# Optimization experiments

Measured on AMD Instinct MI355X. Metric: run time of the kernel, lower is better.

Reference implementation:

```python
import jax, jax.numpy as jnp
import numpy as np

TOP_K = 2
NUM_EXPERTS = 64


def setup_inputs() -> dict:
    key = jax.random.key(0)
    k1, k2 = jax.random.split(key)
    hidden_states = jax.random.normal(k1, (4, 4096, 2048), dtype=jnp.float32)
    gate_weight = jax.random.normal(k2, (NUM_EXPERTS, 2048), dtype=jnp.float32) * 0.02
    return {"hidden_states": hidden_states, "gate_weight": gate_weight}


def reference(hidden_states, gate_weight):
    B, S, D = hidden_states.shape
    E = gate_weight.shape[0]
    num_tokens = B * S
    x = hidden_states.reshape(num_tokens, D)
    # gate: Linear(d_model, num_experts, bias=False)
    gate_logits = jnp.einsum('td,ed->te', x, gate_weight)  # [T, E]
    gate_probs = jax.nn.softmax(gate_logits, axis=-1)
    top_k_probs, top_k_indices = jax.lax.top_k(gate_probs, TOP_K)
    # normalize_gates=True
    top_k_probs = top_k_probs / jnp.sum(top_k_probs, axis=-1, keepdims=True)
    # histogram of expert assignments (replaces the python loop over experts)
    tokens_per_expert = jax.ops.segment_sum(
        jnp.ones((num_tokens * TOP_K,), dtype=jnp.float32),
        top_k_indices.reshape(-1),
        num_segments=E,
    )
    # auxiliary load-balancing loss
    fraction_per_expert = tokens_per_expert / num_tokens
    mean_gate_probs = jnp.mean(gate_probs, axis=0)
    aux_loss = jnp.sum(fraction_per_expert * mean_gate_probs) * E
    return top_k_probs, top_k_indices, tokens_per_expert, aux_loss
```

## Files before the change

kernel.cpp:

```cpp
#include <hip/hip_runtime.h>
#include <hip/hip_bf16.h>

#define TOKENS   16384
#define DMODEL   2048
#define NEXP     64
#define BK       64
#define TB       32
#define TT       8

#define OFF_IDX  (TOKENS * 2)
#define OFF_HIST (TOKENS * 4)
#define OFF_AUX  (TOKENS * 4 + NEXP)

__global__ __launch_bounds__(256) void router_kernel(
    const float* __restrict__ x,
    const float* __restrict__ gw,
    float* __restrict__ out,
    float* __restrict__ probsum_g,
    float* __restrict__ hist_g)
{
    __shared__ float xs[TB][BK];
    __shared__ float wt[BK][NEXP + 1];
    __shared__ float psum_s[4][NEXP];
    __shared__ int   hist_s[NEXP];

    const int tid  = threadIdx.x;
    const int wave = tid >> 6;
    const int lane = tid & 63;
    const int tok0 = blockIdx.x * TB;

    if (tid < NEXP) hist_s[tid] = 0;

    float acc[TT];
#pragma unroll
    for (int t = 0; t < TT; ++t) acc[t] = 0.f;

    for (int k0 = 0; k0 < DMODEL; k0 += BK) {
        __syncthreads();
#pragma unroll
        for (int i = 0; i < (TB * BK / 4) / 256; ++i) {
            int idx = tid + i * 256;
            int r = idx >> 4;
            int c = idx & 15;
            *(float4*)&xs[r][c * 4] =
                *(const float4*)&x[(size_t)(tok0 + r) * DMODEL + k0 + c * 4];
        }
#pragma unroll
        for (int i = 0; i < 4; ++i) {
            int idx = tid + i * 256;
            int e = idx >> 4;
            int c = idx & 15;
            float4 v = *(const float4*)&gw[(size_t)e * DMODEL + k0 + c * 4];
            wt[c * 4 + 0][e] = v.x;
            wt[c * 4 + 1][e] = v.y;
            wt[c * 4 + 2][e] = v.z;
            wt[c * 4 + 3][e] = v.w;
        }
        __syncthreads();

#pragma unroll
        for (int kk4 = 0; kk4 < BK / 4; ++kk4) {
            float w0 = wt[kk4 * 4 + 0][lane];
            float w1 = wt[kk4 * 4 + 1][lane];
            float w2 = wt[kk4 * 4 + 2][lane];
            float w3 = wt[kk4 * 4 + 3][lane];
#pragma unroll
            for (int t = 0; t < TT; ++t) {
                float4 xv = *(const float4*)&xs[wave * TT + t][kk4 * 4];
                acc[t] = fmaf(xv.x, w0, acc[t]);
                acc[t] = fmaf(xv.y, w1, acc[t]);
                acc[t] = fmaf(xv.z, w2, acc[t]);
                acc[t] = fmaf(xv.w, w3, acc[t]);
            }
        }
    }

    float local_psum = 0.f;
    const int tokA = tok0 + wave * TT;

#pragma unroll
    for (int t = 0; t < TT; ++t) {
        float v = acc[t];
        float m = v;
#pragma unroll
        for (int off = 32; off; off >>= 1) m = fmaxf(m, __shfl_xor(m, off));
        float ex = __expf(v - m);
        float S = ex;
#pragma unroll
        for (int off = 32; off; off >>= 1) S += __shfl_xor(S, off);
        local_psum += ex / S;

        float bv = v; int bi = lane;
#pragma unroll
        for (int off = 32; off; off >>= 1) {
            float ov = __shfl_xor(bv, off);
            int   oi = __shfl_xor(bi, off);
            if (ov > bv || (ov == bv && oi < bi)) { bv = ov; bi = oi; }
        }
        float v1 = bv; int i1 = bi;
        float bv2 = (lane == i1) ? -3.4e38f : v; int bi2 = lane;
#pragma unroll
        for (int off = 32; off; off >>= 1) {
            float ov = __shfl_xor(bv2, off);
            int   oi = __shfl_xor(bi2, off);
            if (ov > bv2 || (ov == bv2 && oi < bi2)) { bv2 = ov; bi2 = oi; }
        }
        float v2 = bv2; int i2 = bi2;

        if (lane == 0) {
            float e1 = __expf(v1 - m);
            float e2 = __expf(v2 - m);
            float inv = 1.f / (e1 + e2);
            int tok = tokA + t;
            out[tok * 2 + 0] = e1 * inv;
            out[tok * 2 + 1] = e2 * inv;
            out[OFF_IDX + tok * 2 + 0] = (float)i1;
            out[OFF_IDX + tok * 2 + 1] = (float)i2;
            atomicAdd(&hist_s[i1], 1);
            atomicAdd(&hist_s[i2], 1);
        }
    }

    psum_s[wave][lane] = local_psum;
    __syncthreads();
    if (wave == 0) {
        float s = psum_s[0][lane] + psum_s[1][lane] + psum_s[2][lane] + psum_s[3][lane];
        atomicAdd(&probsum_g[lane], s);
        atomicAdd(&hist_g[lane], (float)hist_s[lane]);
    }
}

__global__ void finalize_kernel(const float* __restrict__ probsum_g,
                                const float* __restrict__ hist_g,
                                float* __restrict__ out)
{
    int e = threadIdx.x;
    float tpe = hist_g[e];
    out[OFF_HIST + e] = tpe;
    const float invT = 1.f / (float)TOKENS;
    float term = (tpe * invT) * (probsum_g[e] * invT);
#pragma unroll
    for (int off = 32; off; off >>= 1) term += __shfl_xor(term, off);
    if (e == 0) out[OFF_AUX] = term * (float)NEXP;
}

extern "C" void kernel_launch(void* const* d_in, const int* in_sizes, int n_in,
                              void* d_out, int out_size, void* d_ws, size_t ws_size,
                              hipStream_t stream) {
    const float* x  = (const float*)d_in[0];
    const float* gw = (const float*)d_in[1];
    float* out = (float*)d_out;
    float* ws  = (float*)d_ws;

    hipMemsetAsync(d_ws, 0, 128 * sizeof(float), stream);

    dim3 grid(TOKENS / TB);
    router_kernel<<<grid, 256, 0, stream>>>(x, gw, out, ws, ws + NEXP);
    finalize_kernel<<<1, 64, 0, stream>>>(ws, ws + NEXP, out);
}
```

Before: 210.8 us.

## Restructure router GEMM: lane-per-token, wave-uniform weight loads, double-buffered x tiles

Each lane now owns a token and each wave owns 8 experts, so gate weights are read as wave-uniform (scalar-friendly) global loads instead of being transposed into shared memory. x tiles of 64 tokens are double-buffered with register prefetch, and logits are transposed through shared memory for the softmax and top-2 stage. Blocks grow to 512 threads with 64 tokens each. This removes the shared-memory weight transpose and cuts LDS traffic per FMA. The cost is per-iteration global weight reads and an extra shared-memory transpose step.

```diff
diff --git a/kernel.cpp b/kernel.cpp
--- a/kernel.cpp
+++ b/kernel.cpp
@@ -4,24 +4,25 @@
 #define TOKENS   16384
 #define DMODEL   2048
 #define NEXP     64
-#define BK       64
-#define TB       32
-#define TT       8
+#define KW       64
+#define NIT      (DMODEL / KW)
+#define TB       64
+#define PAD      68
 
 #define OFF_IDX  (TOKENS * 2)
 #define OFF_HIST (TOKENS * 4)
 #define OFF_AUX  (TOKENS * 4 + NEXP)
 
-__global__ __launch_bounds__(256) void router_kernel(
+__global__ __launch_bounds__(512) void router_kernel(
     const float* __restrict__ x,
     const float* __restrict__ gw,
     float* __restrict__ out,
     float* __restrict__ probsum_g,
     float* __restrict__ hist_g)
 {
-    __shared__ float xs[TB][BK];
-    __shared__ float wt[BK][NEXP + 1];
-    __shared__ float psum_s[4][NEXP];
+    __shared__ float xs[2][TB][PAD];
+    __shared__ float ls[TB][PAD];
+    __shared__ float psum_s[8][NEXP];
     __shared__ int   hist_s[NEXP];
 
     const int tid  = threadIdx.x;
@@ -31,56 +32,66 @@
 
     if (tid < NEXP) hist_s[tid] = 0;
 
-    float acc[TT];
+    const int e0 = __builtin_amdgcn_readfirstlane(wave << 3);
+
+    const float4* wr[8];
 #pragma unroll
-    for (int t = 0; t < TT; ++t) acc[t] = 0.f;
+    for (int j = 0; j < 8; ++j)
+        wr[j] = (const float4*)(gw + (size_t)(e0 + j) * DMODEL);
 
-    for (int k0 = 0; k0 < DMODEL; k0 += BK) {
-        __syncthreads();
+    float acc[8];
 #pragma unroll
-        for (int i = 0; i < (TB * BK / 4) / 256; ++i) {
-            int idx = tid + i * 256;
-            int r = idx >> 4;
-            int c = idx & 15;
-            *(float4*)&xs[r][c * 4] =
-                *(const float4*)&x[(size_t)(tok0 + r) * DMODEL + k0 + c * 4];
-        }
-#pragma unroll
-        for (int i = 0; i < 4; ++i) {
-            int idx = tid + i * 256;
-            int e = idx >> 4;
-            int c = idx & 15;
-            float4 v = *(const float4*)&gw[(size_t)e * DMODEL + k0 + c * 4];
-            wt[c * 4 + 0][e] = v.x;
-            wt[c * 4 + 1][e] = v.y;
-            wt[c * 4 + 2][e] = v.z;
-            wt[c * 4 + 3][e] = v.w;
+    for (int j = 0; j < 8; ++j) acc[j] = 0.f;
+
+    const int sr = tid >> 3;
+    const int sc = (tid & 7) * 8;
+    const float* xrow = x + (size_t)(tok0 + sr) * DMODEL + sc;
+
+    float4 ra = *(const float4*)(xrow);
+    float4 rb = *(const float4*)(xrow + 4);
+    *(float4*)&xs[0][sr][sc]     = ra;
+    *(float4*)&xs[0][sr][sc + 4] = rb;
+    ra = *(const float4*)(xrow + KW);
+    rb = *(const float4*)(xrow + KW + 4);
+
+    for (int it = 0; it < NIT; ++it) {
+        const int cur = it & 1;
+        if (it + 1 < NIT) {
+            *(float4*)&xs[cur ^ 1][sr][sc]     = ra;
+            *(float4*)&xs[cur ^ 1][sr][sc + 4] = rb;
+            if (it + 2 < NIT) {
+                ra = *(const float4*)(xrow + (size_t)(it + 2) * KW);
+                rb = *(const float4*)(xrow + (size_t)(it + 2) * KW + 4);
+            }
         }
         __syncthreads();
 
+        const float* xl = &xs[cur][lane][0];
+        const int kbase = (it * KW) >> 2;
+#pragma unroll 4
+        for (int kk = 0; kk < KW / 4; ++kk) {
+            float4 xv = *(const float4*)(xl + kk * 4);
 #pragma unroll
-        for (int kk4 = 0; kk4 < BK / 4; ++kk4) {
-            float w0 = wt[kk4 * 4 + 0][lane];
-            float w1 = wt[kk4 * 4 + 1][lane];
-            float w2 = wt[kk4 * 4 + 2][lane];
-            float w3 = wt[kk4 * 4 + 3][lane];
-#pragma unroll
-            for (int t = 0; t < TT; ++t) {
-                float4 xv = *(const float4*)&xs[wave * TT + t][kk4 * 4];
-                acc[t] = fmaf(xv.x, w0, acc[t]);
-                acc[t] = fmaf(xv.y, w1, acc[t]);
-                acc[t] = fmaf(xv.z, w2, acc[t]);
-                acc[t] = fmaf(xv.w, w3, acc[t]);
+            for (int j = 0; j < 8; ++j) {
+                float4 wv = wr[j][kbase + kk];
+                acc[j] = fmaf(xv.x, wv.x, acc[j]);
+                acc[j] = fmaf(xv.y, wv.y, acc[j]);
+                acc[j] = fmaf(xv.z, wv.z, acc[j]);
+                acc[j] = fmaf(xv.w, wv.w, acc[j]);
             }
         }
+        __syncthreads();
     }
 
+    *(float4*)&ls[lane][e0]     = make_float4(acc[0], acc[1], acc[2], acc[3]);
+    *(float4*)&ls[lane][e0 + 4] = make_float4(acc[4], acc[5], acc[6], acc[7]);
+    __syncthreads();
+
     float local_psum = 0.f;
-    const int tokA = tok0 + wave * TT;
-
 #pragma unroll
-    for (int t = 0; t < TT; ++t) {
-        float v = acc[t];
+    for (int t = 0; t < 8; ++t) {
+        const int tl = wave * 8 + t;
+        float v = ls[tl][lane];
         float m = v;
 #pragma unroll
         for (int off = 32; off; off >>= 1) m = fmaxf(m, __shfl_xor(m, off));
@@ -111,7 +122,7 @@
             float e1 = __expf(v1 - m);
             float e2 = __expf(v2 - m);
             float inv = 1.f / (e1 + e2);
-            int tok = tokA + t;
+            int tok = tok0 + tl;
             out[tok * 2 + 0] = e1 * inv;
             out[tok * 2 + 1] = e2 * inv;
             out[OFF_IDX + tok * 2 + 0] = (float)i1;
@@ -124,7 +135,9 @@
     psum_s[wave][lane] = local_psum;
     __syncthreads();
     if (wave == 0) {
-        float s = psum_s[0][lane] + psum_s[1][lane] + psum_s[2][lane] + psum_s[3][lane];
+        float s = 0.f;
+#pragma unroll
+        for (int i = 0; i < 8; ++i) s += psum_s[i][lane];
         atomicAdd(&probsum_g[lane], s);
         atomicAdd(&hist_g[lane], (float)hist_s[lane]);
     }
@@ -155,6 +168,6 @@
     hipMemsetAsync(d_ws, 0, 128 * sizeof(float), stream);
 
     dim3 grid(TOKENS / TB);
-    router_kernel<<<grid, 256, 0, stream>>>(x, gw, out, ws, ws + NEXP);
+    router_kernel<<<grid, 512, 0, stream>>>(x, gw, out, ws, ws + NEXP);
     finalize_kernel<<<1, 64, 0, stream>>>(ws, ws + NEXP, out);
 }
```

New measurement: 238.1 us. +12.9%, slower.

## Replace LDS-tiled gate GEMM with register-pipelined direct global loads

Applied to the files above, without the earlier changes.

Removes the shared-memory tiles and per-tile barriers. Each wave now streams its 8 token rows and a per-lane weight column straight from global memory into four rotating register banks, so loads for later chunks are in flight while FMAs run on earlier ones. Scalar prefetch loads touch rows ahead of use, and a separate kernel re-lays the gate weights into a chunk-major layout in workspace so each chunk's weight load is coalesced. This trades LDS traffic and barriers for higher register pressure and broadcast x loads. It also adds an extra kernel launch per call.

```diff
diff --git a/kernel.cpp b/kernel.cpp
--- a/kernel.cpp
+++ b/kernel.cpp
@@ -1,85 +1,146 @@
 #include <hip/hip_runtime.h>
 #include <hip/hip_bf16.h>
 
-#define TOKENS   16384
-#define DMODEL   2048
-#define NEXP     64
-#define BK       64
-#define TB       32
-#define TT       8
+#define TOKENS 16384
+#define DMODEL 2048
+#define NEXP   64
+#define NCH    (DMODEL / 4)
+#define NWIN   32
+#define TPB    32
+#define TPW    8
 
 #define OFF_IDX  (TOKENS * 2)
 #define OFF_HIST (TOKENS * 4)
 #define OFF_AUX  (TOKENS * 4 + NEXP)
 
-__global__ __launch_bounds__(256) void router_kernel(
+#define W4_FLOATS (DMODEL * NEXP)
+
+__global__ __launch_bounds__(256) void transpose_w(const float* __restrict__ gw,
+                                                   float* __restrict__ w4)
+{
+    int idx = blockIdx.x * 256 + threadIdx.x;
+    int e  = idx & 63;
+    int k4 = idx >> 6;
+    float4 v = *(const float4*)(gw + (size_t)e * DMODEL + k4 * 4);
+    *(float4*)(w4 + (size_t)idx * 4) = v;
+}
+
+struct Bank {
+    float4 r0, r1, r2, r3, r4, r5, r6, r7;
+    float4 w;
+};
+
+template<bool USE_W4>
+__global__ __launch_bounds__(256, 2) void router_kernel(
     const float* __restrict__ x,
     const float* __restrict__ gw,
+    const float* __restrict__ w4,
     float* __restrict__ out,
     float* __restrict__ probsum_g,
     float* __restrict__ hist_g)
 {
-    __shared__ float xs[TB][BK];
-    __shared__ float wt[BK][NEXP + 1];
     __shared__ float psum_s[4][NEXP];
     __shared__ int   hist_s[NEXP];
 
     const int tid  = threadIdx.x;
     const int wave = tid >> 6;
     const int lane = tid & 63;
-    const int tok0 = blockIdx.x * TB;
+    const int tko  = __builtin_amdgcn_readfirstlane((int)(blockIdx.x * TPB) + wave * TPW);
 
     if (tid < NEXP) hist_s[tid] = 0;
 
-    float acc[TT];
-#pragma unroll
-    for (int t = 0; t < TT; ++t) acc[t] = 0.f;
-
-    for (int k0 = 0; k0 < DMODEL; k0 += BK) {
-        __syncthreads();
-#pragma unroll
-        for (int i = 0; i < (TB * BK / 4) / 256; ++i) {
-            int idx = tid + i * 256;
-            int r = idx >> 4;
-            int c = idx & 15;
-            *(float4*)&xs[r][c * 4] =
-                *(const float4*)&x[(size_t)(tok0 + r) * DMODEL + k0 + c * 4];
-        }
-#pragma unroll
-        for (int i = 0; i < 4; ++i) {
-            int idx = tid + i * 256;
-            int e = idx >> 4;
-            int c = idx & 15;
-            float4 v = *(const float4*)&gw[(size_t)e * DMODEL + k0 + c * 4];
-            wt[c * 4 + 0][e] = v.x;
-            wt[c * 4 + 1][e] = v.y;
-            wt[c * 4 + 2][e] = v.z;
-            wt[c * 4 + 3][e] = v.w;
-        }
-        __syncthreads();
-
-#pragma unroll
-        for (int kk4 = 0; kk4 < BK / 4; ++kk4) {
-            float w0 = wt[kk4 * 4 + 0][lane];
-            float w1 = wt[kk4 * 4 + 1][lane];
-            float w2 = wt[kk4 * 4 + 2][lane];
-            float w3 = wt[kk4 * 4 + 3][lane];
-#pragma unroll
-            for (int t = 0; t < TT; ++t) {
-                float4 xv = *(const float4*)&xs[wave * TT + t][kk4 * 4];
-                acc[t] = fmaf(xv.x, w0, acc[t]);
-                acc[t] = fmaf(xv.y, w1, acc[t]);
-                acc[t] = fmaf(xv.z, w2, acc[t]);
-                acc[t] = fmaf(xv.w, w3, acc[t]);
-            }
-        }
-    }
+    int lz;
+    asm("v_mov_b32 %0, 0" : "=v"(lz));
+
+    const float* xp0 = x + (size_t)(tko + 0) * DMODEL;
+    const float* xp1 = x + (size_t)(tko + 1) * DMODEL;
+    const float* xp2 = x + (size_t)(tko + 2) * DMODEL;
+    const float* xp3 = x + (size_t)(tko + 3) * DMODEL;
+    const float* xp4 = x + (size_t)(tko + 4) * DMODEL;
+    const float* xp5 = x + (size_t)(tko + 5) * DMODEL;
+    const float* xp6 = x + (size_t)(tko + 6) * DMODEL;
+    const float* xp7 = x + (size_t)(tko + 7) * DMODEL;
+    const float* gwd = gw + (size_t)lane * DMODEL;
+
+    float acc[8];
+#pragma unroll
+    for (int t = 0; t < 8; ++t) acc[t] = 0.f;
+
+    auto LOADB = [&](Bank& B, int C) __attribute__((always_inline)) {
+        B.r0 = *(const float4*)(xp0 + lz + (size_t)C * 4);
+        B.r1 = *(const float4*)(xp1 + lz + (size_t)C * 4);
+        B.r2 = *(const float4*)(xp2 + lz + (size_t)C * 4);
+        B.r3 = *(const float4*)(xp3 + lz + (size_t)C * 4);
+        B.r4 = *(const float4*)(xp4 + lz + (size_t)C * 4);
+        B.r5 = *(const float4*)(xp5 + lz + (size_t)C * 4);
+        B.r6 = *(const float4*)(xp6 + lz + (size_t)C * 4);
+        B.r7 = *(const float4*)(xp7 + lz + (size_t)C * 4);
+        B.w  = USE_W4 ? *(const float4*)(w4 + (size_t)C * (NEXP * 4) + (lane << 2))
+                      : *(const float4*)(gwd + (size_t)C * 4);
+    };
+
+    auto FMAB = [&](Bank& B) __attribute__((always_inline)) {
+        acc[0]=fmaf(B.r0.x,B.w.x,acc[0]); acc[0]=fmaf(B.r0.y,B.w.y,acc[0]);
+        acc[0]=fmaf(B.r0.z,B.w.z,acc[0]); acc[0]=fmaf(B.r0.w,B.w.w,acc[0]);
+        acc[1]=fmaf(B.r1.x,B.w.x,acc[1]); acc[1]=fmaf(B.r1.y,B.w.y,acc[1]);
+        acc[1]=fmaf(B.r1.z,B.w.z,acc[1]); acc[1]=fmaf(B.r1.w,B.w.w,acc[1]);
+        acc[2]=fmaf(B.r2.x,B.w.x,acc[2]); acc[2]=fmaf(B.r2.y,B.w.y,acc[2]);
+        acc[2]=fmaf(B.r2.z,B.w.z,acc[2]); acc[2]=fmaf(B.r2.w,B.w.w,acc[2]);
+        acc[3]=fmaf(B.r3.x,B.w.x,acc[3]); acc[3]=fmaf(B.r3.y,B.w.y,acc[3]);
+        acc[3]=fmaf(B.r3.z,B.w.z,acc[3]); acc[3]=fmaf(B.r3.w,B.w.w,acc[3]);
+        acc[4]=fmaf(B.r4.x,B.w.x,acc[4]); acc[4]=fmaf(B.r4.y,B.w.y,acc[4]);
+        acc[4]=fmaf(B.r4.z,B.w.z,acc[4]); acc[4]=fmaf(B.r4.w,B.w.w,acc[4]);
+        acc[5]=fmaf(B.r5.x,B.w.x,acc[5]); acc[5]=fmaf(B.r5.y,B.w.y,acc[5]);
+        acc[5]=fmaf(B.r5.z,B.w.z,acc[5]); acc[5]=fmaf(B.r5.w,B.w.w,acc[5]);
+        acc[6]=fmaf(B.r6.x,B.w.x,acc[6]); acc[6]=fmaf(B.r6.y,B.w.y,acc[6]);
+        acc[6]=fmaf(B.r6.z,B.w.z,acc[6]); acc[6]=fmaf(B.r6.w,B.w.w,acc[6]);
+        acc[7]=fmaf(B.r7.x,B.w.x,acc[7]); acc[7]=fmaf(B.r7.y,B.w.y,acc[7]);
+        acc[7]=fmaf(B.r7.z,B.w.z,acc[7]); acc[7]=fmaf(B.r7.w,B.w.w,acc[7]);
+    };
+
+    Bank A, B, C, D;
+
+    float pfa = x[(size_t)(tko + (lane >> 3)) * DMODEL + 0 * 64 + ((lane & 3) << 4)];
+    float pfb = x[(size_t)(tko + (lane >> 3)) * DMODEL + 1 * 64 + ((lane & 3) << 4)];
+
+    LOADB(A, 0); LOADB(B, 1); LOADB(C, 2); LOADB(D, 3);
+
+    for (int w = 0; w < NWIN - 1; ++w) {
+        const int c0 = w * 16;
+        float pfn = 0.f;
+        if (w + 2 < NWIN)
+            pfn = x[(size_t)(tko + (lane >> 3)) * DMODEL + (w + 2) * 64 + ((lane & 3) << 4)];
+
+        FMAB(A); LOADB(A, c0 + 4);   FMAB(B); LOADB(B, c0 + 5);
+        FMAB(C); LOADB(C, c0 + 6);   FMAB(D); LOADB(D, c0 + 7);
+        FMAB(A); LOADB(A, c0 + 8);   FMAB(B); LOADB(B, c0 + 9);
+        FMAB(C); LOADB(C, c0 + 10);  FMAB(D); LOADB(D, c0 + 11);
+        FMAB(A); LOADB(A, c0 + 12);  FMAB(B); LOADB(B, c0 + 13);
+        FMAB(C); LOADB(C, c0 + 14);  FMAB(D); LOADB(D, c0 + 15);
+        FMAB(A); LOADB(A, c0 + 16);  FMAB(B); LOADB(B, c0 + 17);
+        FMAB(C); LOADB(C, c0 + 18);  FMAB(D); LOADB(D, c0 + 19);
+
+        asm volatile("" :: "v"(pfa));
+        pfa = pfb; pfb = pfn;
+    }
+    {
+        const int c0 = (NWIN - 1) * 16;
+        FMAB(A); LOADB(A, c0 + 4);   FMAB(B); LOADB(B, c0 + 5);
+        FMAB(C); LOADB(C, c0 + 6);   FMAB(D); LOADB(D, c0 + 7);
+        FMAB(A); LOADB(A, c0 + 8);   FMAB(B); LOADB(B, c0 + 9);
+        FMAB(C); LOADB(C, c0 + 10);  FMAB(D); LOADB(D, c0 + 11);
+        FMAB(A); LOADB(A, c0 + 12);  FMAB(B); LOADB(B, c0 + 13);
+        FMAB(C); LOADB(C, c0 + 14);  FMAB(D); LOADB(D, c0 + 15);
+        FMAB(A); FMAB(B); FMAB(C); FMAB(D);
+        asm volatile("" :: "v"(pfa));
+        asm volatile("" :: "v"(pfb));
+    }
+
+    __syncthreads();
 
     float local_psum = 0.f;
-    const int tokA = tok0 + wave * TT;
-
-#pragma unroll
-    for (int t = 0; t < TT; ++t) {
+#pragma unroll
+    for (int t = 0; t < 8; ++t) {
         float v = acc[t];
         float m = v;
 #pragma unroll
@@ -111,7 +172,7 @@
             float e1 = __expf(v1 - m);
             float e2 = __expf(v2 - m);
             float inv = 1.f / (e1 + e2);
-            int tok = tokA + t;
+            int tok = tko + t;
             out[tok * 2 + 0] = e1 * inv;
             out[tok * 2 + 1] = e2 * inv;
             out[OFF_IDX + tok * 2 + 0] = (float)i1;
@@ -152,9 +213,20 @@
     float* out = (float*)d_out;
     float* ws  = (float*)d_ws;
 
-    hipMemsetAsync(d_ws, 0, 128 * sizeof(float), stream);
-
-    dim3 grid(TOKENS / TB);
-    router_kernel<<<grid, 256, 0, stream>>>(x, gw, out, ws, ws + NEXP);
-    finalize_kernel<<<1, 64, 0, stream>>>(ws, ws + NEXP, out);
-}
+    const bool use_w4 = ws_size >= (size_t)(W4_FLOATS + 128) * sizeof(float);
+    dim3 grid(TOKENS / TPB);
+
+    if (use_w4) {
+        float* w4  = ws;
+        float* acc = ws + W4_FLOATS;
+        (void)hipMemsetAsync(acc, 0, 128 * sizeof(float), stream);
+        transpose_w<<<dim3(128), 256, 0, stream>>>(gw, w4);
+        router_kernel<true><<<grid, 256, 0, stream>>>(x, gw, w4, out, acc, acc + NEXP);
+        finalize_kernel<<<1, 64, 0, stream>>>(acc, acc + NEXP, out);
+    } else {
+        float* acc = ws;
+        (void)hipMemsetAsync(acc, 0, 128 * sizeof(float), stream);
+        router_kernel<false><<<grid, 256, 0, stream>>>(x, gw, nullptr, out, acc, acc + NEXP);
+        finalize_kernel<<<1, 64, 0, stream>>>(acc, acc + NEXP, out);
+    }
+}
```

Result: slower. 386.1 us (+83.1%).
